# Performance work log

Hardware: AMD Instinct MI355X
Metric: run time of the kernel (lower is better)

Reference implementation:

```python
import jax, jax.numpy as jnp
import numpy as np

SCALE = float(np.sqrt(512.0))  # NOTE: module MULTIPLIES by sqrt(dim_attn), not divides


def setup_inputs() -> dict:
    key = jax.random.key(0)
    ks = jax.random.split(key, 10)
    B, N, DQ, DKV, DA = 4, 2048, 512, 512, 512
    w = 0.02  # small init so the *sqrt(d) score scaling stays numerically sane
    return {
        "query": jax.random.normal(ks[0], (B, N, DQ), jnp.float32),
        "key_value": jax.random.normal(ks[1], (B, N, DKV), jnp.float32),
        "Wq": jax.random.normal(ks[2], (DQ, DA), jnp.float32) * w,
        "bq": jnp.zeros((DA,), jnp.float32),
        "Wk": jax.random.normal(ks[3], (DKV, DA), jnp.float32) * w,
        "bk": jnp.zeros((DA,), jnp.float32),
        "Wv": jax.random.normal(ks[4], (DKV, DA), jnp.float32) * w,
        "bv": jnp.zeros((DA,), jnp.float32),
        "Wo": jax.random.normal(ks[5], (DA, DQ), jnp.float32) * w,
        "bo": jnp.zeros((DQ,), jnp.float32),
    }


def reference(query, key_value, Wq, bq, Wk, bk, Wv, bv, Wo, bo):
    # q/k/v projections: (..., dim) @ (dim, dim_attn)
    q = query @ Wq + bq          # [b, nq, da]
    k = key_value @ Wk + bk      # [b, nk, da]
    v = key_value @ Wv + bv      # [b, nk, da]
    # einsum 'dac,dbc->dab' then *sqrt(dim_attn) (faithful: multiply, not divide)
    attn = jnp.einsum('bqc,bkc->bqk', q, k) * SCALE
    attn = jax.nn.softmax(attn, axis=-1)
    # dropout p=0.0 -> no-op
    out = jnp.einsum('bqk,bkc->bqc', attn, v)
    return query + (out @ Wo + bo)
```

## Files before the change

### kernel.cpp

```cpp
#include <hip/hip_runtime.h>

typedef unsigned short u16;
typedef unsigned int u32;
typedef __attribute__((ext_vector_type(8))) __bf16 bf16x8;
typedef __attribute__((ext_vector_type(4))) float f32x4;

#define BK 32

__device__ __forceinline__ u16 f2bf(float x) {
    u32 u = __float_as_uint(x);
    u = (u + 0x7FFFu + ((u >> 16) & 1u)) >> 16;
    return (u16)u;
}
__device__ __forceinline__ float bf2f(u16 h) { return __uint_as_float(((u32)h) << 16); }

#define GLD16(g, l)                                                                        \
    __builtin_amdgcn_global_load_lds((const __attribute__((address_space(1))) void*)(g),   \
                                     (__attribute__((address_space(3))) void*)(l), 16, 0, 0)

template <int N>
__device__ __forceinline__ void vm_wait() {
    if constexpr (N == 0) asm volatile("s_waitcnt vmcnt(0)" ::: "memory");
    else if constexpr (N == 1) asm volatile("s_waitcnt vmcnt(1)" ::: "memory");
    else if constexpr (N == 2) asm volatile("s_waitcnt vmcnt(2)" ::: "memory");
    else if constexpr (N == 3) asm volatile("s_waitcnt vmcnt(3)" ::: "memory");
    else if constexpr (N == 4) asm volatile("s_waitcnt vmcnt(4)" ::: "memory");
    else if constexpr (N == 6) asm volatile("s_waitcnt vmcnt(6)" ::: "memory");
    else if constexpr (N == 8) asm volatile("s_waitcnt vmcnt(8)" ::: "memory");
    else static_assert(N == 0, "unsupported vmcnt literal");
}
#define SBAR() asm volatile("s_barrier" ::: "memory")

__global__ __launch_bounds__(256) void prep_k(
    const float* __restrict__ q, const float* __restrict__ kv,
    u16* __restrict__ QXh, u16* __restrict__ QXl,
    u16* __restrict__ KVh, u16* __restrict__ KVl, long nblk, long n4,
    const float* __restrict__ Wq, const float* __restrict__ Wk,
    const float* __restrict__ Wv, const float* __restrict__ Wo,
    u16* __restrict__ WqTh, u16* __restrict__ WqTl,
    u16* __restrict__ WkvTh, u16* __restrict__ WkvTl,
    u16* __restrict__ WoTh, u16* __restrict__ WoTl, int dim) {
    long b = blockIdx.x;
    if (b < 2 * nblk) {
        const float* x = q; u16* h = QXh; u16* l = QXl;
        if (b >= nblk) { b -= nblk; x = kv; h = KVh; l = KVl; }
        long i = b * 256 + threadIdx.x;
        if (i >= n4) return;
        float4 v = ((const float4*)x)[i];
        float xs[4] = {v.x, v.y, v.z, v.w};
        u16 hh[4], ll[4];
#pragma unroll
        for (int qq = 0; qq < 4; ++qq) {
            hh[qq] = f2bf(xs[qq]);
            ll[qq] = f2bf(xs[qq] - bf2f(hh[qq]));
        }
        uint2 ph, pl;
        ph.x = hh[0] | ((u32)hh[1] << 16); ph.y = hh[2] | ((u32)hh[3] << 16);
        pl.x = ll[0] | ((u32)ll[1] << 16); pl.y = ll[2] | ((u32)ll[3] << 16);
        ((uint2*)h)[i] = ph;
        ((uint2*)l)[i] = pl;
        return;
    }
    long tb = b - 2 * nblk;
    const int z = (int)(tb >> 8);
    const int rem = (int)(tb & 255);
    const long DD = (long)dim * dim;
    const float* W; u16* Th; u16* Tl;
    switch (z) {
        case 0: W = Wq; Th = WqTh; Tl = WqTl; break;
        case 1: W = Wk; Th = WkvTh; Tl = WkvTl; break;
        case 2: W = Wv; Th = WkvTh + DD; Tl = WkvTl + DD; break;
        default: W = Wo; Th = WoTh; Tl = WoTl; break;
    }
    __shared__ float tile[32][33];
    const int bx = (rem & 15) * 32;
    const int by = (rem >> 4) * 32;
    const int tx = threadIdx.x & 31, ty = threadIdx.x >> 5;
    for (int i = 0; i < 32; i += 8)
        tile[ty + i][tx] = W[(size_t)(by + ty + i) * dim + bx + tx];
    __syncthreads();
    for (int i = 0; i < 32; i += 8) {
        float x = tile[tx][ty + i];
        u16 h = f2bf(x);
        size_t idx = (size_t)(bx + ty + i) * dim + by + tx;
        Th[idx] = h;
        Tl[idx] = f2bf(x - bf2f(h));
    }
}

__global__ __launch_bounds__(256) void softmax_k(float* __restrict__ S, int N) {
    float* row = S + (size_t)blockIdx.x * N;
    const int t = threadIdx.x;
    float4 va = ((const float4*)row)[2 * t];
    float4 vb = ((const float4*)row)[2 * t + 1];
    float v[8] = {va.x, va.y, va.z, va.w, vb.x, vb.y, vb.z, vb.w};
    float m = v[0];
#pragma unroll
    for (int i = 1; i < 8; i++) m = fmaxf(m, v[i]);
#pragma unroll
    for (int o = 32; o; o >>= 1) m = fmaxf(m, __shfl_xor(m, o));
    __shared__ float smax[4], ssum[4];
    if ((t & 63) == 0) smax[t >> 6] = m;
    __syncthreads();
    m = fmaxf(fmaxf(smax[0], smax[1]), fmaxf(smax[2], smax[3]));
    float s = 0.f;
#pragma unroll
    for (int i = 0; i < 8; i++) { v[i] = __expf(v[i] - m); s += v[i]; }
#pragma unroll
    for (int o = 32; o; o >>= 1) s += __shfl_xor(s, o);
    if ((t & 63) == 0) ssum[t >> 6] = s;
    __syncthreads();
    s = ssum[0] + ssum[1] + ssum[2] + ssum[3];
    const float inv = 1.0f / s;
    u32 w0 = f2bf(v[0] * inv) | ((u32)f2bf(v[1] * inv) << 16);
    u32 w1 = f2bf(v[2] * inv) | ((u32)f2bf(v[3] * inv) << 16);
    u32 w2 = f2bf(v[4] * inv) | ((u32)f2bf(v[5] * inv) << 16);
    u32 w3 = f2bf(v[6] * inv) | ((u32)f2bf(v[7] * inv) << 16);
    uint4 o4; o4.x = w0; o4.y = w1; o4.z = w2; o4.w = w3;
    ((uint4*)row)[t] = o4;
}

template <int SPLIT, int BMt, int BNt, int WR, int WC>
__global__ __launch_bounds__(256) void gemm_k(
    const u16* __restrict__ Ah, const u16* __restrict__ Al, long lda, long strideA,
    const u16* __restrict__ BTh, const u16* __restrict__ BTl, long ldb, long strideBT,
    const float* __restrict__ bias1, const float* __restrict__ bias2, int nsplit,
    const float* __restrict__ resid, long ldres, float scale,
    float* __restrict__ Cf, long ldcf,
    u16* __restrict__ Cbh, u16* __restrict__ Cbl, long ldcb,
    u16* __restrict__ CbT, long tRows, long tChans, long ldct,
    long strideC, int K) {
    static_assert(WR * WC == 4, "4 waves");
    constexpr int MI = BMt / WR / 16;
    constexpr int NJ = BNt / WC / 16;
    constexpr int PA = BMt / 64;
    constexpr int PB = BNt / 64;
    constexpr int NLD = (PA + PB) * (SPLIT ? 2 : 1);

    __shared__ u16 AsH[2][BMt * BK];
    __shared__ u16 BsH[2][BNt * BK];
    __shared__ u16 AsL[2][(SPLIT ? BMt : 1) * BK];
    __shared__ u16 BsL[2][(SPLIT ? BNt : 1) * BK];

    const long bz = blockIdx.z;
    Ah += bz * strideA;
    BTh += bz * strideBT;
    if constexpr (SPLIT) { Al += bz * strideA; BTl += bz * strideBT; }
    if (Cf) Cf += bz * strideC;
    if (Cbh) Cbh += bz * strideC;
    if (Cbl) Cbl += bz * strideC;

    const int t = threadIdx.x;
    const int w = t >> 6, lane = t & 63;
    const int l15 = lane & 15, quad = lane >> 4;
    const int m0 = blockIdx.x * BMt, n0 = blockIdx.y * BNt;
    const int wrow = (w / WC) * (BMt / WR);
    const int wcol = (w % WC) * (BNt / WC);

    const u16* gAh[PA]; const u16* gAl[PA]; int lA[PA];
    const u16* gBh[PB]; const u16* gBl[PB]; int lB[PB];
#pragma unroll
    for (int p = 0; p < PA; ++p) {
        int slot = p * 256 + t;
        int r = slot >> 2, c = slot & 3;
        int cg = c ^ ((r >> 1) & 3);
        gAh[p] = Ah + (long)(m0 + r) * lda + cg * 8;
        if constexpr (SPLIT) gAl[p] = Al + (long)(m0 + r) * lda + cg * 8;
        lA[p] = (p * 256 + w * 64) * 8;
    }
#pragma unroll
    for (int p = 0; p < PB; ++p) {
        int slot = p * 256 + t;
        int r = slot >> 2, c = slot & 3;
        int cg = c ^ ((r >> 1) & 3);
        gBh[p] = BTh + (long)(n0 + r) * ldb + cg * 8;
        if constexpr (SPLIT) gBl[p] = BTl + (long)(n0 + r) * ldb + cg * 8;
        lB[p] = (p * 256 + w * 64) * 8;
    }

    int aoff[MI], boff[NJ];
#pragma unroll
    for (int i = 0; i < MI; ++i) {
        int r = wrow + i * 16 + l15;
        aoff[i] = (r * 4 + (quad ^ ((r >> 1) & 3))) * 8;
    }
#pragma unroll
    for (int j = 0; j < NJ; ++j) {
        int r = wcol + j * 16 + l15;
        boff[j] = (r * 4 + (quad ^ ((r >> 1) & 3))) * 8;
    }

    f32x4 acc[MI][NJ];
#pragma unroll
    for (int i = 0; i < MI; i++)
#pragma unroll
        for (int j = 0; j < NJ; j++) acc[i][j] = (f32x4){0.f, 0.f, 0.f, 0.f};

    auto stage = [&](int buf) {
#pragma unroll
        for (int p = 0; p < PA; ++p) {
            GLD16(gAh[p], &AsH[buf][lA[p]]);
            gAh[p] += BK;
            if constexpr (SPLIT) { GLD16(gAl[p], &AsL[buf][lA[p]]); gAl[p] += BK; }
        }
#pragma unroll
        for (int p = 0; p < PB; ++p) {
            GLD16(gBh[p], &BsH[buf][lB[p]]);
            gBh[p] += BK;
            if constexpr (SPLIT) { GLD16(gBl[p], &BsL[buf][lB[p]]); gBl[p] += BK; }
        }
    };

    auto compute = [&](int buf) {
        bf16x8 aH[MI], bH[NJ];
#pragma unroll
        for (int i = 0; i < MI; ++i) aH[i] = *(const bf16x8*)&AsH[buf][aoff[i]];
#pragma unroll
        for (int j = 0; j < NJ; ++j) bH[j] = *(const bf16x8*)&BsH[buf][boff[j]];
        if constexpr (SPLIT) {
            bf16x8 aL[MI], bL[NJ];
#pragma unroll
            for (int i = 0; i < MI; ++i) aL[i] = *(const bf16x8*)&AsL[buf][aoff[i]];
#pragma unroll
            for (int j = 0; j < NJ; ++j) bL[j] = *(const bf16x8*)&BsL[buf][boff[j]];
#pragma unroll
            for (int i = 0; i < MI; ++i)
#pragma unroll
                for (int j = 0; j < NJ; ++j) {
                    acc[i][j] = __builtin_amdgcn_mfma_f32_16x16x32_bf16(aH[i], bH[j], acc[i][j], 0, 0, 0);
                    acc[i][j] = __builtin_amdgcn_mfma_f32_16x16x32_bf16(aH[i], bL[j], acc[i][j], 0, 0, 0);
                    acc[i][j] = __builtin_amdgcn_mfma_f32_16x16x32_bf16(aL[i], bH[j], acc[i][j], 0, 0, 0);
                }
        } else {
#pragma unroll
            for (int i = 0; i < MI; ++i)
#pragma unroll
                for (int j = 0; j < NJ; ++j)
                    acc[i][j] = __builtin_amdgcn_mfma_f32_16x16x32_bf16(aH[i], bH[j], acc[i][j], 0, 0, 0);
        }
    };

    const int nt = K / BK;
    stage(0);
    if (nt > 1) stage(1);
    for (int tt = 0; tt < nt; tt += 2) {
        if (tt + 1 < nt) vm_wait<NLD>(); else vm_wait<0>();
        SBAR();
        compute(0);
        SBAR();
        if (tt + 2 < nt) stage(0);
        if (tt + 1 < nt) {
            if (tt + 2 < nt) vm_wait<NLD>(); else vm_wait<0>();
            SBAR();
            compute(1);
            SBAR();
            if (tt + 3 < nt) stage(1);
        }
    }

#pragma unroll
    for (int i = 0; i < MI; ++i) {
#pragma unroll
        for (int j = 0; j < NJ; ++j) {
            const int mBase = m0 + wrow + i * 16 + quad * 4;
            const int nn = n0 + wcol + j * 16 + l15;
            const bool norm = nn < nsplit;
            float bvs;
            if (norm) bvs = bias1 ? bias1[nn] : 0.f;
            else bvs = bias2 ? bias2[nn - nsplit] : 0.f;
#pragma unroll
            for (int r = 0; r < 4; ++r) {
                const long row = mBase + r;
                float x = acc[i][j][r] * scale + bvs;
                if (resid) x += resid[row * ldres + nn];
                if (norm) {
                    if (Cf) Cf[row * ldcf + nn] = x;
                    if (Cbh) {
                        u16 h = f2bf(x);
                        Cbh[row * ldcb + nn] = h;
                        if (Cbl) Cbl[row * ldcb + nn] = f2bf(x - bf2f(h));
                    }
                } else {
                    long b = row / tRows, q = row - b * tRows;
                    CbT[(b * tChans + (nn - nsplit)) * ldct + q] = f2bf(x);
                }
            }
        }
    }
}

extern "C" void kernel_launch(void* const* d_in, const int* in_sizes, int n_in,
                              void* d_out, int out_size, void* d_ws, size_t ws_size,
                              hipStream_t stream) {
    const float* query = (const float*)d_in[0];
    const float* kv    = (const float*)d_in[1];
    const float* Wq = (const float*)d_in[2];
    const float* bq = (const float*)d_in[3];
    const float* Wk = (const float*)d_in[4];
    const float* bk = (const float*)d_in[5];
    const float* Wv = (const float*)d_in[6];
    const float* bv = (const float*)d_in[7];
    const float* Wo = (const float*)d_in[8];
    const float* bo = (const float*)d_in[9];
    float* out = (float*)d_out;

    const int B = 4, N = 2048, D = 512;
    const long MD = (long)B * N * D;
    const int BIG = 1 << 30;

    char* p = (char*)d_ws;
    auto alloc = [&](size_t bytes) { void* r = (void*)p; p += (bytes + 255) & ~(size_t)255; return r; };
    float* S = (float*)alloc((long)B * N * N * 4);
    u16* QXh = (u16*)S;
    u16* QXl = QXh + MD;
    u16* KVh = QXl + MD;
    u16* KVl = KVh + MD;
    u16* Qh = (u16*)alloc(MD * 2);
    u16* Ql = (u16*)alloc(MD * 2);
    u16* Kh = (u16*)alloc(MD * 2);
    u16* Kl = (u16*)alloc(MD * 2);
    u16* Vt = (u16*)alloc(MD * 2);
    u16* Oh = (u16*)alloc(MD * 2);
    u16* WqTh = (u16*)alloc((long)D * D * 2);
    u16* WqTl = (u16*)alloc((long)D * D * 2);
    u16* WkvTh = (u16*)alloc((long)2 * D * D * 2);
    u16* WkvTl = (u16*)alloc((long)2 * D * D * 2);
    u16* WoTh = (u16*)alloc((long)D * D * 2);
    u16* WoTl = (u16*)alloc((long)D * D * 2);

    const dim3 blk(256, 1, 1);
    const float SCALE = 22.627416997969522f;

    prep_k<<<dim3(2 * 4096 + 1024, 1, 1), blk, 0, stream>>>(
        query, kv, QXh, QXl, KVh, KVl, 4096, MD / 4,
        Wq, Wk, Wv, Wo, WqTh, WqTl, WkvTh, WkvTl, WoTh, WoTl, D);

    gemm_k<1, 128, 64, 2, 2><<<dim3(64, 8, 1), blk, 0, stream>>>(
        QXh, QXl, D, 0,
        WqTh, WqTl, D, 0,
        bq, nullptr, BIG,
        nullptr, 0, 1.0f,
        nullptr, 0,
        Qh, Ql, D,
        nullptr, 1, 1, 1,
        0, D);
    gemm_k<1, 128, 64, 2, 2><<<dim3(64, 16, 1), blk, 0, stream>>>(
        KVh, KVl, D, 0,
        WkvTh, WkvTl, D, 0,
        bk, bv, D,
        nullptr, 0, 1.0f,
        nullptr, 0,
        Kh, Kl, D,
        Vt, (long)N, (long)D, (long)N,
        0, D);
    gemm_k<1, 128, 64, 2, 2><<<dim3(16, 32, 4), blk, 0, stream>>>(
        Qh, Ql, D, (long)N * D,
        Kh, Kl, D, (long)N * D,
        nullptr, nullptr, BIG,
        nullptr, 0, SCALE,
        S, N,
        nullptr, nullptr, 0,
        nullptr, 1, 1, 1,
        (long)N * N, D);
    softmax_k<<<dim3(B * N, 1, 1), blk, 0, stream>>>(S, N);
    gemm_k<0, 128, 64, 2, 2><<<dim3(16, 8, 4), blk, 0, stream>>>(
        (const u16*)S, nullptr, 2L * N, (long)N * 2 * N,
        Vt, nullptr, N, (long)D * N,
        nullptr, nullptr, BIG,
        nullptr, 0, 1.0f,
        nullptr, 0,
        Oh, nullptr, D,
        nullptr, 1, 1, 1,
        (long)N * D, N);
    gemm_k<0, 128, 64, 2, 2><<<dim3(64, 8, 1), blk, 0, stream>>>(
        Oh, nullptr, D, 0,
        WoTh, nullptr, D, 0,
        bo, nullptr, BIG,
        query, D, 1.0f,
        out, D,
        nullptr, nullptr, 0,
        nullptr, 1, 1, 1,
        0, D);
    (void)in_sizes; (void)n_in; (void)out_size; (void)ws_size;
}
```

Measured before the change: 334.6 us.

## Merge Q and KV projection launches and overlap next-tile loads with MFMA

```diff
diff --git a/kernel.cpp b/kernel.cpp
--- a/kernel.cpp
+++ b/kernel.cpp
@@ -30,6 +30,7 @@
     else static_assert(N == 0, "unsupported vmcnt literal");
 }
 #define SBAR() asm volatile("s_barrier" ::: "memory")
+#define LGKM0() asm volatile("s_waitcnt lgkmcnt(0)" ::: "memory")
 
 __global__ __launch_bounds__(256) void prep_k(
     const float* __restrict__ q, const float* __restrict__ kv,
@@ -120,16 +121,28 @@
     ((uint4*)row)[t] = o4;
 }
 
+struct GemmArgs {
+    const u16 *Ah, *Al; long lda, strideA;
+    const u16 *BTh, *BTl; long ldb, strideBT;
+    const float *bias1, *bias2; int nsplit;
+    const float* resid; long ldres; float scale;
+    float* Cf; long ldcf;
+    u16 *Cbh, *Cbl; long ldcb;
+    u16* CbT; long tRows, tChans, ldct;
+    long strideC; int K;
+};
+
+template <int SPLIT, int BMt, int BNt>
+struct SmemT {
+    u16 AsH[2][BMt * BK];
+    u16 BsH[2][BNt * BK];
+    u16 AsL[2][(SPLIT ? BMt : 1) * BK];
+    u16 BsL[2][(SPLIT ? BNt : 1) * BK];
+};
+
 template <int SPLIT, int BMt, int BNt, int WR, int WC>
-__global__ __launch_bounds__(256) void gemm_k(
-    const u16* __restrict__ Ah, const u16* __restrict__ Al, long lda, long strideA,
-    const u16* __restrict__ BTh, const u16* __restrict__ BTl, long ldb, long strideBT,
-    const float* __restrict__ bias1, const float* __restrict__ bias2, int nsplit,
-    const float* __restrict__ resid, long ldres, float scale,
-    float* __restrict__ Cf, long ldcf,
-    u16* __restrict__ Cbh, u16* __restrict__ Cbl, long ldcb,
-    u16* __restrict__ CbT, long tRows, long tChans, long ldct,
-    long strideC, int K) {
+__device__ __forceinline__ void gemm_body(SmemT<SPLIT, BMt, BNt>& sm, const GemmArgs& g,
+                                          int bxi, int byi, long bz) {
     static_assert(WR * WC == 4, "4 waves");
     constexpr int MI = BMt / WR / 16;
     constexpr int NJ = BNt / WC / 16;
@@ -137,23 +150,18 @@
     constexpr int PB = BNt / 64;
     constexpr int NLD = (PA + PB) * (SPLIT ? 2 : 1);
 
-    __shared__ u16 AsH[2][BMt * BK];
-    __shared__ u16 BsH[2][BNt * BK];
-    __shared__ u16 AsL[2][(SPLIT ? BMt : 1) * BK];
-    __shared__ u16 BsL[2][(SPLIT ? BNt : 1) * BK];
-
-    const long bz = blockIdx.z;
-    Ah += bz * strideA;
-    BTh += bz * strideBT;
-    if constexpr (SPLIT) { Al += bz * strideA; BTl += bz * strideBT; }
-    if (Cf) Cf += bz * strideC;
-    if (Cbh) Cbh += bz * strideC;
-    if (Cbl) Cbl += bz * strideC;
+    const u16* Ah = g.Ah + bz * g.strideA;
+    const u16* BTh = g.BTh + bz * g.strideBT;
+    const u16* Al = nullptr; const u16* BTl = nullptr;
+    if constexpr (SPLIT) { Al = g.Al + bz * g.strideA; BTl = g.BTl + bz * g.strideBT; }
+    float* Cf = g.Cf ? g.Cf + bz * g.strideC : nullptr;
+    u16* Cbh = g.Cbh ? g.Cbh + bz * g.strideC : nullptr;
+    u16* Cbl = g.Cbl ? g.Cbl + bz * g.strideC : nullptr;
 
     const int t = threadIdx.x;
     const int w = t >> 6, lane = t & 63;
     const int l15 = lane & 15, quad = lane >> 4;
-    const int m0 = blockIdx.x * BMt, n0 = blockIdx.y * BNt;
+    const int m0 = bxi * BMt, n0 = byi * BNt;
     const int wrow = (w / WC) * (BMt / WR);
     const int wcol = (w % WC) * (BNt / WC);
 
@@ -164,8 +172,8 @@
         int slot = p * 256 + t;
         int r = slot >> 2, c = slot & 3;
         int cg = c ^ ((r >> 1) & 3);
-        gAh[p] = Ah + (long)(m0 + r) * lda + cg * 8;
-        if constexpr (SPLIT) gAl[p] = Al + (long)(m0 + r) * lda + cg * 8;
+        gAh[p] = Ah + (long)(m0 + r) * g.lda + cg * 8;
+        if constexpr (SPLIT) gAl[p] = Al + (long)(m0 + r) * g.lda + cg * 8;
         lA[p] = (p * 256 + w * 64) * 8;
     }
 #pragma unroll
@@ -173,8 +181,8 @@
         int slot = p * 256 + t;
         int r = slot >> 2, c = slot & 3;
         int cg = c ^ ((r >> 1) & 3);
-        gBh[p] = BTh + (long)(n0 + r) * ldb + cg * 8;
-        if constexpr (SPLIT) gBl[p] = BTl + (long)(n0 + r) * ldb + cg * 8;
+        gBh[p] = BTh + (long)(n0 + r) * g.ldb + cg * 8;
+        if constexpr (SPLIT) gBl[p] = BTl + (long)(n0 + r) * g.ldb + cg * 8;
         lB[p] = (p * 256 + w * 64) * 8;
     }
 
@@ -199,30 +207,36 @@
     auto stage = [&](int buf) {
 #pragma unroll
         for (int p = 0; p < PA; ++p) {
-            GLD16(gAh[p], &AsH[buf][lA[p]]);
+            GLD16(gAh[p], &sm.AsH[buf][lA[p]]);
             gAh[p] += BK;
-            if constexpr (SPLIT) { GLD16(gAl[p], &AsL[buf][lA[p]]); gAl[p] += BK; }
+            if constexpr (SPLIT) { GLD16(gAl[p], &sm.AsL[buf][lA[p]]); gAl[p] += BK; }
         }
 #pragma unroll
         for (int p = 0; p < PB; ++p) {
-            GLD16(gBh[p], &BsH[buf][lB[p]]);
+            GLD16(gBh[p], &sm.BsH[buf][lB[p]]);
             gBh[p] += BK;
-            if constexpr (SPLIT) { GLD16(gBl[p], &BsL[buf][lB[p]]); gBl[p] += BK; }
+            if constexpr (SPLIT) { GLD16(gBl[p], &sm.BsL[buf][lB[p]]); gBl[p] += BK; }
         }
     };
 
-    auto compute = [&](int buf) {
-        bf16x8 aH[MI], bH[NJ];
-#pragma unroll
-        for (int i = 0; i < MI; ++i) aH[i] = *(const bf16x8*)&AsH[buf][aoff[i]];
-#pragma unroll
-        for (int j = 0; j < NJ; ++j) bH[j] = *(const bf16x8*)&BsH[buf][boff[j]];
+    bf16x8 aH[MI], bH[NJ];
+    bf16x8 aL[SPLIT ? MI : 1], bL[SPLIT ? NJ : 1];
+
+    auto read_frags = [&](int buf) {
+#pragma unroll
+        for (int i = 0; i < MI; ++i) aH[i] = *(const bf16x8*)&sm.AsH[buf][aoff[i]];
+#pragma unroll
+        for (int j = 0; j < NJ; ++j) bH[j] = *(const bf16x8*)&sm.BsH[buf][boff[j]];
         if constexpr (SPLIT) {
-            bf16x8 aL[MI], bL[NJ];
-#pragma unroll
-            for (int i = 0; i < MI; ++i) aL[i] = *(const bf16x8*)&AsL[buf][aoff[i]];
-#pragma unroll
-            for (int j = 0; j < NJ; ++j) bL[j] = *(const bf16x8*)&BsL[buf][boff[j]];
+#pragma unroll
+            for (int i = 0; i < MI; ++i) aL[i] = *(const bf16x8*)&sm.AsL[buf][aoff[i]];
+#pragma unroll
+            for (int j = 0; j < NJ; ++j) bL[j] = *(const bf16x8*)&sm.BsL[buf][boff[j]];
+        }
+    };
+
+    auto mfma_all = [&]() {
+        if constexpr (SPLIT) {
 #pragma unroll
             for (int i = 0; i < MI; ++i)
 #pragma unroll
@@ -240,21 +254,31 @@
         }
     };
 
-    const int nt = K / BK;
+    const int nt = g.K / BK;
     stage(0);
     if (nt > 1) stage(1);
     for (int tt = 0; tt < nt; tt += 2) {
         if (tt + 1 < nt) vm_wait<NLD>(); else vm_wait<0>();
         SBAR();
-        compute(0);
+        read_frags(0);
+        LGKM0();
         SBAR();
         if (tt + 2 < nt) stage(0);
+        __builtin_amdgcn_sched_barrier(0);
+        __builtin_amdgcn_s_setprio(1);
+        mfma_all();
+        __builtin_amdgcn_s_setprio(0);
         if (tt + 1 < nt) {
             if (tt + 2 < nt) vm_wait<NLD>(); else vm_wait<0>();
             SBAR();
-            compute(1);
+            read_frags(1);
+            LGKM0();
             SBAR();
             if (tt + 3 < nt) stage(1);
+            __builtin_amdgcn_sched_barrier(0);
+            __builtin_amdgcn_s_setprio(1);
+            mfma_all();
+            __builtin_amdgcn_s_setprio(0);
         }
     }
 
@@ -264,29 +288,44 @@
         for (int j = 0; j < NJ; ++j) {
             const int mBase = m0 + wrow + i * 16 + quad * 4;
             const int nn = n0 + wcol + j * 16 + l15;
-            const bool norm = nn < nsplit;
+            const bool norm = nn < g.nsplit;
             float bvs;
-            if (norm) bvs = bias1 ? bias1[nn] : 0.f;
-            else bvs = bias2 ? bias2[nn - nsplit] : 0.f;
+            if (norm) bvs = g.bias1 ? g.bias1[nn] : 0.f;
+            else bvs = g.bias2 ? g.bias2[nn - g.nsplit] : 0.f;
 #pragma unroll
             for (int r = 0; r < 4; ++r) {
                 const long row = mBase + r;
-                float x = acc[i][j][r] * scale + bvs;
-                if (resid) x += resid[row * ldres + nn];
+                float x = acc[i][j][r] * g.scale + bvs;
+                if (g.resid) x += g.resid[row * g.ldres + nn];
                 if (norm) {
-                    if (Cf) Cf[row * ldcf + nn] = x;
+                    if (Cf) Cf[row * g.ldcf + nn] = x;
                     if (Cbh) {
                         u16 h = f2bf(x);
-                        Cbh[row * ldcb + nn] = h;
-                        if (Cbl) Cbl[row * ldcb + nn] = f2bf(x - bf2f(h));
+                        Cbh[row * g.ldcb + nn] = h;
+                        if (Cbl) Cbl[row * g.ldcb + nn] = f2bf(x - bf2f(h));
                     }
                 } else {
-                    long b = row / tRows, q = row - b * tRows;
-                    CbT[(b * tChans + (nn - nsplit)) * ldct + q] = f2bf(x);
+                    long b = row / g.tRows, qq = row - b * g.tRows;
+                    g.CbT[(b * g.tChans + (nn - g.nsplit)) * g.ldct + qq] = f2bf(x);
                 }
             }
         }
     }
+}
+
+template <int SPLIT, int BMt, int BNt, int WR, int WC>
+__global__ __launch_bounds__(256) void gemm_k(GemmArgs g) {
+    __shared__ SmemT<SPLIT, BMt, BNt> sm;
+    gemm_body<SPLIT, BMt, BNt, WR, WC>(sm, g, blockIdx.x, blockIdx.y, blockIdx.z);
+}
+
+template <int SPLIT, int BMt, int BNt, int WR, int WC>
+__global__ __launch_bounds__(256) void gemm2_k(GemmArgs g0, int ny0, GemmArgs g1) {
+    __shared__ SmemT<SPLIT, BMt, BNt> sm;
+    if ((int)blockIdx.y < ny0)
+        gemm_body<SPLIT, BMt, BNt, WR, WC>(sm, g0, blockIdx.x, blockIdx.y, blockIdx.z);
+    else
+        gemm_body<SPLIT, BMt, BNt, WR, WC>(sm, g1, blockIdx.x, blockIdx.y - ny0, blockIdx.z);
 }
 
 extern "C" void kernel_launch(void* const* d_in, const int* in_sizes, int n_in,
@@ -335,51 +374,61 @@
         query, kv, QXh, QXl, KVh, KVl, 4096, MD / 4,
         Wq, Wk, Wv, Wo, WqTh, WqTl, WkvTh, WkvTl, WoTh, WoTl, D);
 
-    gemm_k<1, 128, 64, 2, 2><<<dim3(64, 8, 1), blk, 0, stream>>>(
-        QXh, QXl, D, 0,
-        WqTh, WqTl, D, 0,
-        bq, nullptr, BIG,
-        nullptr, 0, 1.0f,
-        nullptr, 0,
-        Qh, Ql, D,
-        nullptr, 1, 1, 1,
-        0, D);
-    gemm_k<1, 128, 64, 2, 2><<<dim3(64, 16, 1), blk, 0, stream>>>(
-        KVh, KVl, D, 0,
-        WkvTh, WkvTl, D, 0,
-        bk, bv, D,
-        nullptr, 0, 1.0f,
-        nullptr, 0,
-        Kh, Kl, D,
-        Vt, (long)N, (long)D, (long)N,
-        0, D);
-    gemm_k<1, 128, 64, 2, 2><<<dim3(16, 32, 4), blk, 0, stream>>>(
-        Qh, Ql, D, (long)N * D,
-        Kh, Kl, D, (long)N * D,
-        nullptr, nullptr, BIG,
-        nullptr, 0, SCALE,
-        S, N,
-        nullptr, nullptr, 0,
-        nullptr, 1, 1, 1,
-        (long)N * N, D);
+    GemmArgs qa{};
+    qa.Ah = QXh; qa.Al = QXl; qa.lda = D; qa.strideA = 0;
+    qa.BTh = WqTh; qa.BTl = WqTl; qa.ldb = D; qa.strideBT = 0;
+    qa.bias1 = bq; qa.bias2 = nullptr; qa.nsplit = BIG;
+    qa.resid = nullptr; qa.ldres = 0; qa.scale = 1.0f;
+    qa.Cf = nullptr; qa.ldcf = 0;
+    qa.Cbh = Qh; qa.Cbl = Ql; qa.ldcb = D;
+    qa.CbT = nullptr; qa.tRows = 1; qa.tChans = 1; qa.ldct = 1;
+    qa.strideC = 0; qa.K = D;
+
+    GemmArgs ka{};
+    ka.Ah = KVh; ka.Al = KVl; ka.lda = D; ka.strideA = 0;
+    ka.BTh = WkvTh; ka.BTl = WkvTl; ka.ldb = D; ka.strideBT = 0;
+    ka.bias1 = bk; ka.bias2 = bv; ka.nsplit = D;
+    ka.resid = nullptr; ka.ldres = 0; ka.scale = 1.0f;
+    ka.Cf = nullptr; ka.ldcf = 0;
+    ka.Cbh = Kh; ka.Cbl = Kl; ka.ldcb = D;
+    ka.CbT = Vt; ka.tRows = N; ka.tChans = D; ka.ldct = N;
+    ka.strideC = 0; ka.K = D;
+    gemm2_k<1, 128, 64, 2, 2><<<dim3(64, 24, 1), blk, 0, stream>>>(qa, 8, ka);
+
+    GemmArgs sa{};
+    sa.Ah = Qh; sa.Al = Ql; sa.lda = D; sa.strideA = (long)N * D;
+    sa.BTh = Kh; sa.BTl = Kl; sa.ldb = D; sa.strideBT = (long)N * D;
+    sa.bias1 = nullptr; sa.bias2 = nullptr; sa.nsplit = BIG;
+    sa.resid = nullptr; sa.ldres = 0; sa.scale = SCALE;
+    sa.Cf = S; sa.ldcf = N;
+    sa.Cbh = nullptr; sa.Cbl = nullptr; sa.ldcb = 0;
+    sa.CbT = nullptr; sa.tRows = 1; sa.tChans = 1; sa.ldct = 1;
+    sa.strideC = (long)N * N; sa.K = D;
+    gemm_k<1, 128, 64, 2, 2><<<dim3(16, 32, 4), blk, 0, stream>>>(sa);
+
     softmax_k<<<dim3(B * N, 1, 1), blk, 0, stream>>>(S, N);
-    gemm_k<0, 128, 64, 2, 2><<<dim3(16, 8, 4), blk, 0, stream>>>(
-        (const u16*)S, nullptr, 2L * N, (long)N * 2 * N,
-        Vt, nullptr, N, (long)D * N,
-        nullptr, nullptr, BIG,
-        nullptr, 0, 1.0f,
-        nullptr, 0,
-        Oh, nullptr, D,
-        nullptr, 1, 1, 1,
-        (long)N * D, N);
-    gemm_k<0, 128, 64, 2, 2><<<dim3(64, 8, 1), blk, 0, stream>>>(
-        Oh, nullptr, D, 0,
-        WoTh, nullptr, D, 0,
-        bo, nullptr, BIG,
-        query, D, 1.0f,
-        out, D,
-        nullptr, nullptr, 0,
-        nullptr, 1, 1, 1,
-        0, D);
+
+    GemmArgs pa{};
+    pa.Ah = (const u16*)S; pa.Al = nullptr; pa.lda = 2L * N; pa.strideA = (long)N * 2 * N;
+    pa.BTh = Vt; pa.BTl = nullptr; pa.ldb = N; pa.strideBT = (long)D * N;
+    pa.bias1 = nullptr; pa.bias2 = nullptr; pa.nsplit = BIG;
+    pa.resid = nullptr; pa.ldres = 0; pa.scale = 1.0f;
+    pa.Cf = nullptr; pa.ldcf = 0;
+    pa.Cbh = Oh; pa.Cbl = nullptr; pa.ldcb = D;
+    pa.CbT = nullptr; pa.tRows = 1; pa.tChans = 1; pa.ldct = 1;
+    pa.strideC = (long)N * D; pa.K = N;
+    gemm_k<0, 128, 64, 2, 2><<<dim3(16, 8, 4), blk, 0, stream>>>(pa);
+
+    GemmArgs oa{};
+    oa.Ah = Oh; oa.Al = nullptr; oa.lda = D; oa.strideA = 0;
+    oa.BTh = WoTh; oa.BTl = nullptr; oa.ldb = D; oa.strideBT = 0;
+    oa.bias1 = bo; oa.bias2 = nullptr; oa.nsplit = BIG;
+    oa.resid = query; oa.ldres = D; oa.scale = 1.0f;
+    oa.Cf = out; oa.ldcf = D;
+    oa.Cbh = nullptr; oa.Cbl = nullptr; oa.ldcb = 0;
+    oa.CbT = nullptr; oa.tRows = 1; oa.tChans = 1; oa.ldct = 1;
+    oa.strideC = 0; oa.K = D;
+    gemm_k<0, 128, 64, 2, 2><<<dim3(64, 8, 1), blk, 0, stream>>>(oa);
+
     (void)in_sizes; (void)n_in; (void)out_size; (void)ws_size;
 }
```

Measured after the change: 372.5 us. 11.3% more time.
